# Kernel tuning notes

Measured on AMD Instinct MI355X. Metric: run time of the kernel, lower is better.

Reference implementation:

```python
import jax, jax.numpy as jnp
import numpy as np

P_DROP = 0.25
DROP_KEY_SEED = 42  # fixed seed makes dropout deterministic for baseline comparison


def setup_inputs() -> dict:
    key = jax.random.key(0)
    k1, k2, k3, k4 = jax.random.split(key, 4)
    B, S, D, DV = 16, 2048, 64, 512
    x1 = jax.random.normal(k1, (B, S, D), dtype=jnp.float32)   # queries [B,S,64]
    m = jax.random.normal(k2, (D, DV), dtype=jnp.float32)      # [64,512]
    n = jax.random.normal(k3, (S, DV), dtype=jnp.float32)      # [S,512]
    q = jax.random.normal(k4, (S, DV), dtype=jnp.float32)      # values [S,512]
    return {"x1": x1, "m": m, "n": n, "q": q}


def reference(x1, m, n, q):
    scale = jnp.float32(1.0 / 64.0)  # hard-coded in original (not 1/sqrt(d))
    kT = jnp.matmul(m, n.T)                        # matmul5: [64, S]
    scores = jnp.matmul(x1, kT) * scale            # [B, S, S]
    probs = jax.nn.softmax(scores, axis=-1)        # softmax over last dim
    keep = jax.random.bernoulli(jax.random.key(DROP_KEY_SEED), 1.0 - P_DROP, probs.shape)
    probs = jnp.where(keep, probs / (1.0 - P_DROP), jnp.float32(0.0))  # dropout (train mode)
    return jnp.matmul(probs, q)                    # [B, S, DV]
```

## Files before the change

kernel.cpp:

```cpp
#include <hip/hip_runtime.h>


typedef short  s8v __attribute__((ext_vector_type(8)));
typedef float  f4v __attribute__((ext_vector_type(4)));

__device__ __forceinline__ unsigned short f2bf(float f) {
  unsigned int u = __float_as_uint(f);
  u += 0x7fffu + ((u >> 16) & 1u);
  return (unsigned short)(u >> 16);
}
__device__ __forceinline__ float bf2f(unsigned short h) {
  return __uint_as_float(((unsigned int)h) << 16);
}
__device__ __forceinline__ unsigned int pack_bf2(float a, float b) {
  unsigned int ua = __float_as_uint(a);
  ua += 0x7fffu + ((ua >> 16) & 1u);
  unsigned int ub = __float_as_uint(b);
  ub += 0x7fffu + ((ub >> 16) & 1u);
  return (ua >> 16) | (ub & 0xffff0000u);
}

__device__ __forceinline__ unsigned int rotl(unsigned int x, unsigned int r) {
  return __builtin_amdgcn_alignbit(x, x, 32u - r);
}

__device__ __forceinline__ unsigned int jax_bits(unsigned int idx) {
  const unsigned int K0 = 0u, K1 = 42u, K2 = 0x1BD11BDAu ^ K0 ^ K1;
  unsigned int x0 = 0u, x1 = idx;
  x0 += K0; x1 += K1;
#define TF_R(r) { x0 += x1; x1 = rotl(x1, r); x1 ^= x0; }
  TF_R(13) TF_R(15) TF_R(26) TF_R(6)
  x0 += K1; x1 += K2 + 1u;
  TF_R(17) TF_R(29) TF_R(16) TF_R(24)
  x0 += K2; x1 += K0 + 2u;
  TF_R(13) TF_R(15) TF_R(26) TF_R(6)
  x0 += K0; x1 += K1 + 3u;
  TF_R(17) TF_R(29) TF_R(16) TF_R(24)
  x0 += K1; x1 += K2 + 4u;
  TF_R(13) TF_R(15) TF_R(26) TF_R(6)
  x0 += K2; x1 += K0 + 5u;
#undef TF_R
  return x0 ^ x1;
}

__device__ __forceinline__ f4v mfma16(s8v a, s8v b, f4v c) {
  return __builtin_amdgcn_mfma_f32_16x16x32_bf16(a, b, c, 0, 0, 0);
}

__global__ void prep_misc(const float* __restrict__ x1, const float* __restrict__ q,
                          const float* __restrict__ m,
                          unsigned short* __restrict__ Xhi,
                          unsigned short* __restrict__ qT,
                          float* __restrict__ mT) {
  const int blk = blockIdx.x;
  const int t = threadIdx.x;
  if (blk < 1024) {
    const int i = (blk * 256 + t) * 8;
    float4 a = *(const float4*)&x1[i];
    float4 b = *(const float4*)&x1[i + 4];
    ushort4 o0, o1;
    o0.x = f2bf(a.x); o0.y = f2bf(a.y); o0.z = f2bf(a.z); o0.w = f2bf(a.w);
    o1.x = f2bf(b.x); o1.y = f2bf(b.y); o1.z = f2bf(b.z); o1.w = f2bf(b.w);
    *(ushort4*)&Xhi[i] = o0;
    *(ushort4*)&Xhi[i + 4] = o1;
  } else if (blk < 1280) {
    __shared__ unsigned short tile[64][65];
    const int bb = blk - 1024;
    const int s0 = (bb >> 3) * 64;
    const int d0 = (bb & 7) * 64;
#pragma unroll
    for (int k = 0; k < 16; ++k) {
      int lin = t + k * 256;
      int r = lin >> 6, c = lin & 63;
      tile[c][r] = f2bf(q[(size_t)(s0 + r) * 512 + d0 + c]);
    }
    __syncthreads();
#pragma unroll
    for (int k = 0; k < 16; ++k) {
      int lin = t + k * 256;
      int rr = lin >> 6, cc = lin & 63;
      qT[(size_t)(d0 + rr) * 2048 + s0 + cc] = tile[rr][cc];
    }
  } else {
    const int i = (blk - 1280) * 256 + t;
    int dv = i >> 6, d = i & 63;
    mT[i] = m[d * 512 + dv];
  }
}

__global__ void build_k(const float* __restrict__ mT, const float* __restrict__ n,
                        unsigned short* __restrict__ Khi, unsigned short* __restrict__ Klo) {
  const int s = blockIdx.x * 4 + (threadIdx.x >> 6);
  const int d = threadIdx.x & 63;
  const float* nrow = n + (size_t)s * 512;
  float a0 = 0.f, a1 = 0.f, a2 = 0.f, a3 = 0.f;
  for (int dv = 0; dv < 512; dv += 4) {
    a0 = fmaf(mT[(dv + 0) * 64 + d], nrow[dv + 0], a0);
    a1 = fmaf(mT[(dv + 1) * 64 + d], nrow[dv + 1], a1);
    a2 = fmaf(mT[(dv + 2) * 64 + d], nrow[dv + 2], a2);
    a3 = fmaf(mT[(dv + 3) * 64 + d], nrow[dv + 3], a3);
  }
  float k = ((a0 + a1) + (a2 + a3)) * 0.015625f;
  unsigned short h = f2bf(k);
  Khi[s * 64 + d] = h;
  Klo[s * 64 + d] = f2bf(k - bf2f(h));
}

__global__ __launch_bounds__(512, 4) void attn_main(
    const unsigned short* __restrict__ Xhi,
    const unsigned short* __restrict__ Khi, const unsigned short* __restrict__ Klo,
    const unsigned short* __restrict__ qT, float* __restrict__ out) {
  __shared__ unsigned short Ks[2][128][72];
  __shared__ unsigned short Ps[64][136];
  __shared__ float rsum[2][64];

  const int tid  = threadIdx.x;
  const int wave = tid >> 6;
  const int lane = tid & 63;
  const int l15  = lane & 15;
  const int quad = lane >> 4;

  const int b    = blockIdx.x >> 5;
  const int row0 = (blockIdx.x & 31) * 64;

  const int qk_row = (wave & 3) * 16 + l15;
  const int qk_kg  = (wave >> 2) * 64;

  const size_t xg = ((size_t)(b * 2048 + row0 + qk_row)) * 64 + quad * 8;
  const s8v X0 = *(const s8v*)&Xhi[xg];
  const s8v X1 = *(const s8v*)&Xhi[xg + 32];

  f4v acc[4][4];
#pragma unroll
  for (int mt = 0; mt < 4; ++mt)
#pragma unroll
    for (int nt = 0; nt < 4; ++nt) acc[mt][nt] = f4v{0.f, 0.f, 0.f, 0.f};
  float rs = 0.f;

  const unsigned int idx_row =
      ((unsigned int)(b * 2048 + row0 + qk_row)) * 2048u;

  for (int it = 0; it < 16; ++it) {
    const int kt = it * 128;
    __syncthreads();
    {
      const int kk = tid >> 2, c = (tid & 3) * 16;
      const size_t g = ((size_t)(kt + kk)) * 64 + c;
      *(uint4*)&Ks[0][kk][c]     = *(const uint4*)&Khi[g];
      *(uint4*)&Ks[0][kk][c + 8] = *(const uint4*)&Khi[g + 8];
      *(uint4*)&Ks[1][kk][c]     = *(const uint4*)&Klo[g];
      *(uint4*)&Ks[1][kk][c + 8] = *(const uint4*)&Klo[g + 8];
    }
    __syncthreads();

#pragma unroll
    for (int nt = 0; nt < 4; ++nt) {
      const int key = qk_kg + nt * 16 + l15;
      s8v Kh0 = *(const s8v*)&Ks[0][key][quad * 8];
      s8v Kh1 = *(const s8v*)&Ks[0][key][32 + quad * 8];
      s8v Kl0 = *(const s8v*)&Ks[1][key][quad * 8];
      s8v Kl1 = *(const s8v*)&Ks[1][key][32 + quad * 8];
      f4v c = {0.f, 0.f, 0.f, 0.f};
      c = mfma16(Kh0, X0, c);  c = mfma16(Kh1, X1, c);
      c = mfma16(Kl0, X0, c);  c = mfma16(Kl1, X1, c);
      const unsigned int idx0 = idx_row + (unsigned int)(kt + qk_kg + nt * 16 + quad * 4);
      float p[4];
#pragma unroll
      for (int r = 0; r < 4; ++r) {
        float e = __expf(c[r]);
        rs += e;
        const unsigned int bits = jax_bits(idx0 + r);
        p[r] = (bits < 0xC0000000u) ? e : 0.0f;
      }
      const unsigned int p01 = pack_bf2(p[0], p[1]);
      const unsigned int p23 = pack_bf2(p[2], p[3]);
      *(uint2*)&Ps[(wave & 3) * 16 + l15][qk_kg + nt * 16 + quad * 4] =
          make_uint2(p01, p23);
    }
    __syncthreads();

#pragma unroll
    for (int ks = 0; ks < 4; ++ks) {
      s8v Va[4];
#pragma unroll
      for (int mt = 0; mt < 4; ++mt) {
        const size_t g =
            (size_t)(wave * 64 + mt * 16 + l15) * 2048 + kt + ks * 32 + quad * 8;
        Va[mt] = *(const s8v*)&qT[g];
      }
#pragma unroll
      for (int nt = 0; nt < 4; ++nt) {
        s8v Pb = *(const s8v*)&Ps[nt * 16 + l15][ks * 32 + quad * 8];
#pragma unroll
        for (int mt = 0; mt < 4; ++mt) acc[mt][nt] = mfma16(Va[mt], Pb, acc[mt][nt]);
      }
    }
  }

  {
    float v = rs;
    v += __shfl_xor(v, 16);
    v += __shfl_xor(v, 32);
    if (quad == 0) rsum[wave >> 2][(wave & 3) * 16 + l15] = v;
  }
  __syncthreads();

#pragma unroll
  for (int nt = 0; nt < 4; ++nt) {
    const int rloc = nt * 16 + l15;
    const int row = row0 + rloc;
    const float inv = 1.0f / (0.75f * (rsum[0][rloc] + rsum[1][rloc]));
    const size_t base = ((size_t)(b * 2048 + row)) * 512 + wave * 64;
#pragma unroll
    for (int mt = 0; mt < 4; ++mt) {
      f4v v = acc[mt][nt];
      v[0] *= inv; v[1] *= inv; v[2] *= inv; v[3] *= inv;
      *(f4v*)&out[base + mt * 16 + quad * 4] = v;
    }
  }
}

extern "C" void kernel_launch(void* const* d_in, const int* in_sizes, int n_in,
                              void* d_out, int out_size, void* d_ws, size_t ws_size,
                              hipStream_t stream) {
  (void)in_sizes; (void)n_in; (void)out_size; (void)ws_size;
  const float* x1 = (const float*)d_in[0];
  const float* m  = (const float*)d_in[1];
  const float* n  = (const float*)d_in[2];
  const float* q  = (const float*)d_in[3];
  float* out = (float*)d_out;

  char* ws = (char*)d_ws;
  float*          mT  = (float*)(ws + 0);
  unsigned short* Khi = (unsigned short*)(ws + 131072);
  unsigned short* Klo = (unsigned short*)(ws + 393216);
  unsigned short* Xhi = (unsigned short*)(ws + 655360);
  unsigned short* qT  = (unsigned short*)(ws + 4849664);

  prep_misc<<<1408, 256, 0, stream>>>(x1, q, m, Xhi, qT, mT);
  build_k<<<512, 256, 0, stream>>>(mT, n, Khi, Klo);
  attn_main<<<512, 512, 0, stream>>>(Xhi, Khi, Klo, qT, out);
}
```

Measured before the change: 321.4 us.

## Drop K low-part split, software-pipeline QK/PV with double-buffered P, fuse m transpose

Removes the bf16 hi/lo split of K, so QK^T uses two MFMAs per tile instead of four and K is read straight from global memory instead of being staged in LDS. The main loop is restructured so the QK and dropout/exp of iteration it overlaps the PV of iteration it-1, using a double-buffered P tile and one barrier per iteration. build_k now transposes m through an LDS tile itself, removing the separate mT pass, and packing uses the HIP bf16x2 conversion. Dropping Klo lowers score precision, which may push results closer to the tolerance.

New measurement: 410.5 us. 1.28x slower.

```diff
diff --git a/kernel.cpp b/kernel.cpp
--- a/kernel.cpp
+++ b/kernel.cpp
@@ -1,4 +1,5 @@
 #include <hip/hip_runtime.h>
+#include <hip/hip_bf16.h>
 
 
 typedef short  s8v __attribute__((ext_vector_type(8)));
@@ -9,15 +10,11 @@
   u += 0x7fffu + ((u >> 16) & 1u);
   return (unsigned short)(u >> 16);
 }
-__device__ __forceinline__ float bf2f(unsigned short h) {
-  return __uint_as_float(((unsigned int)h) << 16);
-}
 __device__ __forceinline__ unsigned int pack_bf2(float a, float b) {
-  unsigned int ua = __float_as_uint(a);
-  ua += 0x7fffu + ((ua >> 16) & 1u);
-  unsigned int ub = __float_as_uint(b);
-  ub += 0x7fffu + ((ub >> 16) & 1u);
-  return (ua >> 16) | (ub & 0xffff0000u);
+  __hip_bfloat162 h = __float22bfloat162_rn(float2{a, b});
+  unsigned int u;
+  __builtin_memcpy(&u, &h, 4);
+  return u;
 }
 
 __device__ __forceinline__ unsigned int rotl(unsigned int x, unsigned int r) {
@@ -48,10 +45,8 @@
 }
 
 __global__ void prep_misc(const float* __restrict__ x1, const float* __restrict__ q,
-                          const float* __restrict__ m,
                           unsigned short* __restrict__ Xhi,
-                          unsigned short* __restrict__ qT,
-                          float* __restrict__ mT) {
+                          unsigned short* __restrict__ qT) {
   const int blk = blockIdx.x;
   const int t = threadIdx.x;
   if (blk < 1024) {
@@ -63,7 +58,7 @@
     o1.x = f2bf(b.x); o1.y = f2bf(b.y); o1.z = f2bf(b.z); o1.w = f2bf(b.w);
     *(ushort4*)&Xhi[i] = o0;
     *(ushort4*)&Xhi[i + 4] = o1;
-  } else if (blk < 1280) {
+  } else {
     __shared__ unsigned short tile[64][65];
     const int bb = blk - 1024;
     const int s0 = (bb >> 3) * 64;
@@ -81,37 +76,50 @@
       int rr = lin >> 6, cc = lin & 63;
       qT[(size_t)(d0 + rr) * 2048 + s0 + cc] = tile[rr][cc];
     }
-  } else {
-    const int i = (blk - 1280) * 256 + t;
-    int dv = i >> 6, d = i & 63;
-    mT[i] = m[d * 512 + dv];
-  }
-}
-
-__global__ void build_k(const float* __restrict__ mT, const float* __restrict__ n,
-                        unsigned short* __restrict__ Khi, unsigned short* __restrict__ Klo) {
-  const int s = blockIdx.x * 4 + (threadIdx.x >> 6);
-  const int d = threadIdx.x & 63;
-  const float* nrow = n + (size_t)s * 512;
+  }
+}
+
+__global__ __launch_bounds__(256) void build_k(const float* __restrict__ m,
+                                               const float* __restrict__ n,
+                                               unsigned short* __restrict__ Khi) {
+  __shared__ float tile[32][65];
+  const int t = threadIdx.x;
+  const int d = t & 63;
+  const int w = t >> 6;
+  const int s0 = blockIdx.x * 16;
+  const int ld_d = t >> 2;
+  const int ld_c = (t & 3) * 8;
   float a0 = 0.f, a1 = 0.f, a2 = 0.f, a3 = 0.f;
-  for (int dv = 0; dv < 512; dv += 4) {
-    a0 = fmaf(mT[(dv + 0) * 64 + d], nrow[dv + 0], a0);
-    a1 = fmaf(mT[(dv + 1) * 64 + d], nrow[dv + 1], a1);
-    a2 = fmaf(mT[(dv + 2) * 64 + d], nrow[dv + 2], a2);
-    a3 = fmaf(mT[(dv + 3) * 64 + d], nrow[dv + 3], a3);
-  }
-  float k = ((a0 + a1) + (a2 + a3)) * 0.015625f;
-  unsigned short h = f2bf(k);
-  Khi[s * 64 + d] = h;
-  Klo[s * 64 + d] = f2bf(k - bf2f(h));
+  for (int c0 = 0; c0 < 512; c0 += 32) {
+    __syncthreads();
+    float4 va = *(const float4*)&m[ld_d * 512 + c0 + ld_c];
+    float4 vb = *(const float4*)&m[ld_d * 512 + c0 + ld_c + 4];
+    tile[ld_c + 0][ld_d] = va.x; tile[ld_c + 1][ld_d] = va.y;
+    tile[ld_c + 2][ld_d] = va.z; tile[ld_c + 3][ld_d] = va.w;
+    tile[ld_c + 4][ld_d] = vb.x; tile[ld_c + 5][ld_d] = vb.y;
+    tile[ld_c + 6][ld_d] = vb.z; tile[ld_c + 7][ld_d] = vb.w;
+    __syncthreads();
+    const float* n0 = &n[(size_t)(s0 + w * 4 + 0) * 512 + c0];
+    const float* n1 = &n[(size_t)(s0 + w * 4 + 1) * 512 + c0];
+    const float* n2 = &n[(size_t)(s0 + w * 4 + 2) * 512 + c0];
+    const float* n3 = &n[(size_t)(s0 + w * 4 + 3) * 512 + c0];
+#pragma unroll
+    for (int j = 0; j < 32; ++j) {
+      float mv = tile[j][d];
+      a0 = fmaf(mv, n0[j], a0); a1 = fmaf(mv, n1[j], a1);
+      a2 = fmaf(mv, n2[j], a2); a3 = fmaf(mv, n3[j], a3);
+    }
+  }
+  Khi[(s0 + w * 4 + 0) * 64 + d] = f2bf(a0 * 0.015625f);
+  Khi[(s0 + w * 4 + 1) * 64 + d] = f2bf(a1 * 0.015625f);
+  Khi[(s0 + w * 4 + 2) * 64 + d] = f2bf(a2 * 0.015625f);
+  Khi[(s0 + w * 4 + 3) * 64 + d] = f2bf(a3 * 0.015625f);
 }
 
 __global__ __launch_bounds__(512, 4) void attn_main(
-    const unsigned short* __restrict__ Xhi,
-    const unsigned short* __restrict__ Khi, const unsigned short* __restrict__ Klo,
+    const unsigned short* __restrict__ Xhi, const unsigned short* __restrict__ Khi,
     const unsigned short* __restrict__ qT, float* __restrict__ out) {
-  __shared__ unsigned short Ks[2][128][72];
-  __shared__ unsigned short Ps[64][136];
+  __shared__ unsigned short Ps[2][64][152];
   __shared__ float rsum[2][64];
 
   const int tid  = threadIdx.x;
@@ -140,62 +148,71 @@
   const unsigned int idx_row =
       ((unsigned int)(b * 2048 + row0 + qk_row)) * 2048u;
 
-  for (int it = 0; it < 16; ++it) {
+  auto qk_phase = [&](int it, f4v cf[4]) {
     const int kt = it * 128;
-    __syncthreads();
-    {
-      const int kk = tid >> 2, c = (tid & 3) * 16;
-      const size_t g = ((size_t)(kt + kk)) * 64 + c;
-      *(uint4*)&Ks[0][kk][c]     = *(const uint4*)&Khi[g];
-      *(uint4*)&Ks[0][kk][c + 8] = *(const uint4*)&Khi[g + 8];
-      *(uint4*)&Ks[1][kk][c]     = *(const uint4*)&Klo[g];
-      *(uint4*)&Ks[1][kk][c + 8] = *(const uint4*)&Klo[g + 8];
-    }
-    __syncthreads();
-
 #pragma unroll
     for (int nt = 0; nt < 4; ++nt) {
-      const int key = qk_kg + nt * 16 + l15;
-      s8v Kh0 = *(const s8v*)&Ks[0][key][quad * 8];
-      s8v Kh1 = *(const s8v*)&Ks[0][key][32 + quad * 8];
-      s8v Kl0 = *(const s8v*)&Ks[1][key][quad * 8];
-      s8v Kl1 = *(const s8v*)&Ks[1][key][32 + quad * 8];
+      const int key = kt + qk_kg + nt * 16 + l15;
+      const s8v Ka = *(const s8v*)&Khi[key * 64 + quad * 8];
+      const s8v Kb = *(const s8v*)&Khi[key * 64 + 32 + quad * 8];
       f4v c = {0.f, 0.f, 0.f, 0.f};
-      c = mfma16(Kh0, X0, c);  c = mfma16(Kh1, X1, c);
-      c = mfma16(Kl0, X0, c);  c = mfma16(Kl1, X1, c);
-      const unsigned int idx0 = idx_row + (unsigned int)(kt + qk_kg + nt * 16 + quad * 4);
+      c = mfma16(Ka, X0, c);
+      cf[nt] = mfma16(Kb, X1, c);
+    }
+  };
+  auto tf_phase = [&](int it, f4v cf[4]) {
+    const int kt = it * 128;
+    const int buf = it & 1;
+#pragma unroll
+    for (int nt = 0; nt < 4; ++nt) {
+      const unsigned int idx0 =
+          idx_row + (unsigned int)(kt + qk_kg + nt * 16 + quad * 4);
       float p[4];
 #pragma unroll
       for (int r = 0; r < 4; ++r) {
-        float e = __expf(c[r]);
+        float e = __expf(cf[nt][r]);
         rs += e;
-        const unsigned int bits = jax_bits(idx0 + r);
-        p[r] = (bits < 0xC0000000u) ? e : 0.0f;
+        p[r] = (jax_bits(idx0 + r) < 0xC0000000u) ? e : 0.0f;
       }
-      const unsigned int p01 = pack_bf2(p[0], p[1]);
-      const unsigned int p23 = pack_bf2(p[2], p[3]);
-      *(uint2*)&Ps[(wave & 3) * 16 + l15][qk_kg + nt * 16 + quad * 4] =
-          make_uint2(p01, p23);
-    }
-    __syncthreads();
-
+      *(uint2*)&Ps[buf][(wave & 3) * 16 + l15][qk_kg + nt * 16 + quad * 4] =
+          make_uint2(pack_bf2(p[0], p[1]), pack_bf2(p[2], p[3]));
+    }
+  };
+  auto pv_phase = [&](int it) {
+    const int kt = it * 128;
+    const int buf = it & 1;
 #pragma unroll
     for (int ks = 0; ks < 4; ++ks) {
       s8v Va[4];
 #pragma unroll
-      for (int mt = 0; mt < 4; ++mt) {
-        const size_t g =
-            (size_t)(wave * 64 + mt * 16 + l15) * 2048 + kt + ks * 32 + quad * 8;
-        Va[mt] = *(const s8v*)&qT[g];
+      for (int mt = 0; mt < 4; ++mt)
+        Va[mt] = *(const s8v*)&qT[(size_t)(wave * 64 + mt * 16 + l15) * 2048 +
+                                  kt + ks * 32 + quad * 8];
+#pragma unroll
+      for (int nt = 0; nt < 4; ++nt) {
+        const s8v Pb = *(const s8v*)&Ps[buf][nt * 16 + l15][ks * 32 + quad * 8];
+#pragma unroll
+        for (int mt = 0; mt < 4; ++mt)
+          acc[mt][nt] = mfma16(Va[mt], Pb, acc[mt][nt]);
       }
-#pragma unroll
-      for (int nt = 0; nt < 4; ++nt) {
-        s8v Pb = *(const s8v*)&Ps[nt * 16 + l15][ks * 32 + quad * 8];
-#pragma unroll
-        for (int mt = 0; mt < 4; ++mt) acc[mt][nt] = mfma16(Va[mt], Pb, acc[mt][nt]);
-      }
-    }
-  }
+    }
+  };
+
+  {
+    f4v cf[4];
+    qk_phase(0, cf);
+    tf_phase(0, cf);
+  }
+  __syncthreads();
+#pragma unroll 2
+  for (int it = 1; it < 16; ++it) {
+    f4v cf[4];
+    qk_phase(it, cf);
+    pv_phase(it - 1);
+    tf_phase(it, cf);
+    __syncthreads();
+  }
+  pv_phase(15);
 
   {
     float v = rs;
@@ -231,13 +248,11 @@
   float* out = (float*)d_out;
 
   char* ws = (char*)d_ws;
-  float*          mT  = (float*)(ws + 0);
-  unsigned short* Khi = (unsigned short*)(ws + 131072);
-  unsigned short* Klo = (unsigned short*)(ws + 393216);
-  unsigned short* Xhi = (unsigned short*)(ws + 655360);
-  unsigned short* qT  = (unsigned short*)(ws + 4849664);
-
-  prep_misc<<<1408, 256, 0, stream>>>(x1, q, m, Xhi, qT, mT);
-  build_k<<<512, 256, 0, stream>>>(mT, n, Khi, Klo);
-  attn_main<<<512, 512, 0, stream>>>(Xhi, Khi, Klo, qT, out);
-}
+  unsigned short* Khi = (unsigned short*)(ws + 0);
+  unsigned short* Xhi = (unsigned short*)(ws + 262144);
+  unsigned short* qT  = (unsigned short*)(ws + 4456448);
+
+  prep_misc<<<1280, 256, 0, stream>>>(x1, q, Xhi, qT);
+  build_k<<<128, 256, 0, stream>>>(m, n, Khi);
+  attn_main<<<512, 512, 0, stream>>>(Xhi, Khi, qT, out);
+}
```
